# Performance work log

Hardware: AMD Instinct MI355X
Metric: run time of the kernel (lower is better)

The kernel has to match this reference:

```python
import jax, jax.numpy as jnp
import numpy as np

N = 100_000   # nodes
E = 1_600_000 # edges
F = 128       # num_node_features
H = 128       # hidden_channels
C = 10        # num_classes
G = 128       # graphs in batch


def setup_inputs() -> dict:
    key = jax.random.key(0)
    ks = jax.random.split(key, 12)
    x = jax.random.normal(ks[0], (N, F), jnp.float32)
    edge_index = jax.random.randint(ks[1], (2, E), 0, N, dtype=jnp.int32)
    batch = jnp.sort(jax.random.randint(ks[2], (N,), 0, G, dtype=jnp.int32))
    s = 1.0 / np.sqrt(H)
    W0 = jax.random.normal(ks[3], (F, H), jnp.float32) * s
    b0 = jnp.zeros((H,), jnp.float32)
    W1 = jax.random.normal(ks[4], (H, H), jnp.float32) * s
    b1 = jnp.zeros((H,), jnp.float32)
    W2 = jax.random.normal(ks[5], (H, H), jnp.float32) * s
    b2 = jnp.zeros((H,), jnp.float32)
    Wlin = jax.random.normal(ks[6], (H, C), jnp.float32) * s
    blin = jnp.zeros((C,), jnp.float32)
    return {"x": x, "edge_index": edge_index, "batch": batch,
            "W0": W0, "b0": b0, "W1": W1, "b1": b1, "W2": W2, "b2": b2,
            "Wlin": Wlin, "blin": blin}


def gcn_conv(x, W, b, src, dst):
    """PyG GCNConv: symmetric-normalized aggregation with self-loops."""
    xw = x @ W  # [N, H]
    # degree from destination column, +1 for self-loop (gcn_norm)
    deg = jax.ops.segment_sum(jnp.ones(src.shape[0], xw.dtype), dst,
                              num_segments=N) + 1.0
    dinv = jax.lax.rsqrt(deg)  # deg^{-1/2}
    # edge messages: xw[src] * deg_src^{-1/2} * deg_dst^{-1/2}
    msg = xw[src] * (dinv[src] * dinv[dst])[:, None]  # [E, H]
    agg = jax.ops.segment_sum(msg, dst, num_segments=N)
    # self-loop contribution: xw * deg^{-1}
    return agg + xw * (dinv * dinv)[:, None] + b


def reference(x, edge_index, batch, W0, b0, W1, b1, W2, b2, Wlin, blin):
    src, dst = edge_index[0], edge_index[1]
    h = jax.nn.relu(gcn_conv(x, W0, b0, src, dst))
    h = jax.nn.relu(gcn_conv(h, W1, b1, src, dst))
    h = jax.nn.relu(gcn_conv(h, W2, b2, src, dst))
    # global_mean_pool over graph ids
    cnt = jax.ops.segment_sum(jnp.ones(N, h.dtype), batch, num_segments=G)
    pooled = jax.ops.segment_sum(h, batch, num_segments=G) / jnp.maximum(cnt, 1.0)[:, None]
    # dropout is identity in eval mode
    return pooled @ Wlin + blin  # [G, C]
```

## Files before the change

kernel.cpp:

```cpp
#include <hip/hip_runtime.h>

typedef short short8 __attribute__((ext_vector_type(8)));
typedef float f32x4 __attribute__((ext_vector_type(4)));
typedef float f32x2 __attribute__((ext_vector_type(2)));

#define HDIM 128
#define SCAN_NB 256
#define SCAN_TPB 256
#define XCC_GETREG_IMM (20 | (31 << 11))

__device__ __forceinline__ ushort f2bf(float f) {
  uint u = __float_as_uint(f);
  u += 0x7fffu + ((u >> 16) & 1u);
  return (ushort)(u >> 16);
}
__device__ __forceinline__ float bflo(uint v){ return __uint_as_float(v << 16); }
__device__ __forceinline__ float bfhi(uint v){ return __uint_as_float(v & 0xffff0000u); }
__device__ __forceinline__ uchar f2fp8(float f) {
  int p = __builtin_amdgcn_cvt_pk_fp8_f32(f, f, 0, false);
  return (uchar)(p & 0xff);
}

__global__ __launch_bounds__(256) void k_wconv(const float* __restrict__ W0, const float* __restrict__ W1,
    const float* __restrict__ W2, ushort* __restrict__ wf) {
  int b = blockIdx.x;
  const float* W = (b < 8) ? W0 : (b < 16) ? W1 : W2;
  ushort* out = wf + (size_t)(b >> 3) * 16384;
  int g = (b & 7) * 256 + threadIdx.x;
  int nt = g >> 8, kc = (g >> 6) & 3, lane = g & 63;
  int colB = lane & 15, krow = (lane >> 4) * 8;
  ushort v[8];
  #pragma unroll
  for (int j = 0; j < 8; ++j)
    v[j] = f2bf(W[(kc*32 + krow + j)*HDIM + nt*16 + colB]);
  #pragma unroll
  for (int j = 0; j < 8; ++j) out[(size_t)g*8 + j] = v[j];
}

__global__ __launch_bounds__(256) void k_deg(const int* __restrict__ dst, int E, int N,
                                             int* __restrict__ degc8, ushort* __restrict__ rank) {
  uint xcd = __builtin_amdgcn_s_getreg(XCC_GETREG_IMM) & 7u;
  int* plane = degc8 + (size_t)xcd * N;
  for (int e = blockIdx.x*blockDim.x + threadIdx.x; e < E; e += gridDim.x*blockDim.x) {
    int d = dst[e];
    int r = __hip_atomic_fetch_add(&plane[d], 1, __ATOMIC_RELAXED, __HIP_MEMORY_SCOPE_WORKGROUP);
    rank[e] = (ushort)((xcd << 13) | (uint)r);
  }
}

__global__ __launch_bounds__(SCAN_TPB) void k_scanA(const int* __restrict__ degc8, int N,
    int* __restrict__ degc, int* __restrict__ blocksum, float* __restrict__ dinv) {
  int ipt = (N + SCAN_NB*SCAN_TPB - 1) / (SCAN_NB*SCAN_TPB);
  int chunk = ipt * SCAN_TPB;
  int start = blockIdx.x * chunk + threadIdx.x * ipt;
  int s = 0;
  #pragma unroll
  for (int k = 0; k < 4; ++k) {
    if (k < ipt) {
      int i = start + k;
      if (i < N) {
        int d = 0;
        #pragma unroll
        for (int x = 0; x < 8; ++x) d += degc8[(size_t)x*N + i];
        degc[i] = d;
        s += d;
        dinv[i] = rsqrtf((float)d + 1.0f);
      }
    }
  }
  __shared__ int red[SCAN_TPB];
  int t = threadIdx.x;
  red[t] = s; __syncthreads();
  for (int off = SCAN_TPB/2; off > 0; off >>= 1) {
    if (t < off) red[t] += red[t+off];
    __syncthreads();
  }
  if (t == 0) blocksum[blockIdx.x] = red[0];
}

__global__ __launch_bounds__(SCAN_NB) void k_scanB(const int* __restrict__ blocksum,
    int* __restrict__ blockoff, int* __restrict__ totalN,
    const int* __restrict__ batch, int N, int G, float* __restrict__ inv_cnt) {
  int t = threadIdx.x;
  if (blockIdx.x == 0) {
    __shared__ int sh[SCAN_NB];
    sh[t] = blocksum[t];
    __syncthreads();
    for (int off = 1; off < SCAN_NB; off <<= 1) {
      int v = (t >= off) ? sh[t-off] : 0;
      __syncthreads();
      sh[t] += v;
      __syncthreads();
    }
    blockoff[t] = (t == 0) ? 0 : sh[t-1];
    if (t == SCAN_NB-1) *totalN = sh[t];
  } else {
    __shared__ int bnd[SCAN_NB+1];
    if (t <= G) {
      int lo = 0, hi = N;
      while (lo < hi) { int mid = (lo + hi) >> 1; if (batch[mid] < t) lo = mid + 1; else hi = mid; }
      bnd[t] = lo;
    }
    __syncthreads();
    if (t < G) {
      int c = bnd[t+1] - bnd[t];
      inv_cnt[t] = 1.0f / (float)max(c, 1);
    }
  }
}

__global__ __launch_bounds__(SCAN_TPB) void k_scanC(const int* __restrict__ degc,
    const int* __restrict__ degc8, int N,
    const int* __restrict__ blockoff, const int* __restrict__ totalN,
    int* __restrict__ row_ptr, int* __restrict__ row_ptr8) {
  int ipt = (N + SCAN_NB*SCAN_TPB - 1) / (SCAN_NB*SCAN_TPB);
  int chunk = ipt * SCAN_TPB;
  int start = blockIdx.x * chunk + threadIdx.x * ipt;
  int t = threadIdx.x;
  int vals[4];
  int s = 0;
  #pragma unroll
  for (int k = 0; k < 4; ++k) {
    int v = 0;
    if (k < ipt) { int i = start + k; if (i < N) v = degc[i]; }
    vals[k] = v; s += v;
  }
  __shared__ int sh[SCAN_TPB];
  sh[t] = s; __syncthreads();
  for (int off = 1; off < SCAN_TPB; off <<= 1) {
    int v = (t >= off) ? sh[t-off] : 0;
    __syncthreads();
    sh[t] += v;
    __syncthreads();
  }
  int run = blockoff[blockIdx.x] + ((t == 0) ? 0 : sh[t-1]);
  #pragma unroll
  for (int k = 0; k < 4; ++k) {
    if (k < ipt) {
      int i = start + k;
      if (i < N) {
        row_ptr[i] = run;
        int c = run;
        #pragma unroll
        for (int x = 0; x < 8; ++x) {
          row_ptr8[(size_t)x*N + i] = c;
          c += degc8[(size_t)x*N + i];
        }
      }
    }
    run += vals[k];
  }
  if (blockIdx.x == 0 && t == 0) row_ptr[N] = *totalN;
}

__global__ __launch_bounds__(256) void k_fill(const int* __restrict__ src, const int* __restrict__ dst, int E, int N,
    const float* __restrict__ dinv, const int* __restrict__ row_ptr8, const ushort* __restrict__ rank,
    int2* __restrict__ epack) {
  for (int e = blockIdx.x*blockDim.x + threadIdx.x; e < E; e += gridDim.x*blockDim.x) {
    int s = src[e], d = dst[e];
    uint rk = rank[e];
    uint xcd = rk >> 13;
    int  r   = (int)(rk & 0x1FFFu);
    int pos = row_ptr8[(size_t)xcd*N + d] + r;
    float cf = dinv[s] * dinv[d];
    epack[pos] = make_int2(s, __float_as_int(cf));
  }
}

template<int IN_F32>
__global__ __launch_bounds__(256,1) void k_gemm(const void* __restrict__ in_, const ushort* __restrict__ wf,
    uchar* __restrict__ xw8, int N) {
  int lane = threadIdx.x & 63;
  int wid  = (blockIdx.x * blockDim.x + threadIdx.x) >> 6;
  int nw   = (gridDim.x * blockDim.x) >> 6;
  int colB = lane & 15;
  int krow = (lane >> 4) * 8;

  short8 bfr[8][4];
  #pragma unroll
  for (int nt = 0; nt < 8; ++nt)
    #pragma unroll
    for (int kc = 0; kc < 4; ++kc)
      bfr[nt][kc] = *(const short8*)(wf + (((nt<<2) + kc) << 9) + (lane << 3));

  int strips = (N + 15) >> 4;
  for (int s = wid; s < strips; s += nw) {
    int ra = s*16 + colB;
    bool va = ra < N;
    short8 a[4];
    if (IN_F32) {
      const float* xin = (const float*)in_;
      #pragma unroll
      for (int kc = 0; kc < 4; ++kc) {
        short8 t = {0,0,0,0,0,0,0,0};
        if (va) {
          const float* p = xin + (size_t)ra*HDIM + kc*32 + krow;
          float4 lo4 = *(const float4*)p;
          float4 hi4 = *(const float4*)(p+4);
          t[0]=(short)f2bf(lo4.x); t[1]=(short)f2bf(lo4.y); t[2]=(short)f2bf(lo4.z); t[3]=(short)f2bf(lo4.w);
          t[4]=(short)f2bf(hi4.x); t[5]=(short)f2bf(hi4.y); t[6]=(short)f2bf(hi4.z); t[7]=(short)f2bf(hi4.w);
        }
        a[kc] = t;
      }
    } else {
      const ushort* hin = (const ushort*)in_;
      #pragma unroll
      for (int kc = 0; kc < 4; ++kc) {
        short8 t = {0,0,0,0,0,0,0,0};
        if (va) t = *(const short8*)(hin + (size_t)ra*HDIM + kc*32 + krow);
        a[kc] = t;
      }
    }
    f32x4 acc[8];
    #pragma unroll
    for (int nt = 0; nt < 8; ++nt) { acc[nt][0]=0.f; acc[nt][1]=0.f; acc[nt][2]=0.f; acc[nt][3]=0.f; }
    #pragma unroll
    for (int nt = 0; nt < 8; ++nt)
      #pragma unroll
      for (int kc = 0; kc < 4; ++kc)
        acc[nt] = __builtin_amdgcn_mfma_f32_16x16x32_bf16(a[kc], bfr[nt][kc], acc[nt], 0, 0, 0);

    int r0 = s*16 + (lane>>4)*4;
    #pragma unroll
    for (int nt = 0; nt < 8; ++nt) {
      int c = nt*16 + colB;
      #pragma unroll
      for (int rg = 0; rg < 4; ++rg) {
        int rr = r0 + rg;
        if (rr < N) xw8[(size_t)rr*HDIM + c] = f2fp8(acc[nt][rg]);
      }
    }
  }
}

__global__ __launch_bounds__(256) void k_agg(const ushort* __restrict__ xw8u, const int2* __restrict__ epack,
    const int* __restrict__ row_ptr, const float* __restrict__ dinv, const float* __restrict__ bias,
    uint* __restrict__ hu, int N) {
  int lane = threadIdx.x & 63;
  int n = blockIdx.x*4 + (threadIdx.x >> 6);
  if (n >= N) return;
  int e0 = row_ptr[n], e1 = row_ptr[n+1];
  float a0 = 0.f, a1 = 0.f;
  for (int base = e0; base < e1; base += 64) {
    int cnt = min(64, e1 - base);
    int2 myp = make_int2(0, 0);
    if (lane < cnt) myp = epack[base + lane];
    for (int j = 0; j < cnt; j += 16) {
      #pragma unroll
      for (int u = 0; u < 16; ++u) {
        int idx = j + u;
        int   sN = __shfl(myp.x, idx);
        float cf = __int_as_float(__shfl(myp.y, idx));
        int v16 = (int)xw8u[(size_t)sN*64 + lane];
        f32x2 f = __builtin_amdgcn_cvt_pk_f32_fp8(v16, false);
        a0 += cf * f[0];
        a1 += cf * f[1];
      }
    }
  }
  float di = dinv[n]; float w = di*di;
  int v16s = (int)xw8u[(size_t)n*64 + lane];
  f32x2 fs = __builtin_amdgcn_cvt_pk_f32_fp8(v16s, false);
  a0 += w * fs[0];
  a1 += w * fs[1];
  a0 += bias[lane*2];  a1 += bias[lane*2+1];
  a0 = fmaxf(a0, 0.f); a1 = fmaxf(a1, 0.f);
  uint o = ((uint)f2bf(a0)) | (((uint)f2bf(a1)) << 16);
  hu[(size_t)n*64 + lane] = o;
}

__global__ __launch_bounds__(256) void k_pool(const uint* __restrict__ hu, const int* __restrict__ batch,
    float* __restrict__ psum, int N) {
  int lane = threadIdx.x & 63;
  int wave = threadIdx.x >> 6;
  int n0 = blockIdx.x*512 + wave*128;
  if (n0 >= N) return;
  int n1 = min(n0 + 128, N);
  float a0 = 0.f, a1 = 0.f;
  int gc = batch[n0];
  for (int n = n0; n < n1; ++n) {
    int g = batch[n];
    if (g != gc) {
      atomicAdd(&psum[gc*HDIM + lane*2],   a0);
      atomicAdd(&psum[gc*HDIM + lane*2+1], a1);
      a0 = 0.f; a1 = 0.f; gc = g;
    }
    uint v = hu[(size_t)n*64 + lane];
    a0 += bflo(v); a1 += bfhi(v);
  }
  atomicAdd(&psum[gc*HDIM + lane*2],   a0);
  atomicAdd(&psum[gc*HDIM + lane*2+1], a1);
}

__global__ __launch_bounds__(256) void k_final(const float* __restrict__ psum, const float* __restrict__ inv_cnt,
    const float* __restrict__ Wlin, const float* __restrict__ blin, float* __restrict__ out, int G, int C) {
  int idx = blockIdx.x*256 + threadIdx.x;
  if (idx >= G*C) return;
  int g = idx / C, c = idx % C;
  float acc = 0.f;
  for (int k = 0; k < HDIM; ++k) acc += psum[g*HDIM + k] * Wlin[k*C + c];
  out[idx] = acc * inv_cnt[g] + blin[c];
}

extern "C" void kernel_launch(void* const* d_in, const int* in_sizes, int n_in,
                              void* d_out, int out_size, void* d_ws, size_t ws_size,
                              hipStream_t stream) {
  const float* x    = (const float*)d_in[0];
  const int*   ei   = (const int*)d_in[1];
  const int*   batch= (const int*)d_in[2];
  const float* W0   = (const float*)d_in[3];
  const float* b0   = (const float*)d_in[4];
  const float* W1   = (const float*)d_in[5];
  const float* b1   = (const float*)d_in[6];
  const float* W2   = (const float*)d_in[7];
  const float* b2   = (const float*)d_in[8];
  const float* Wlin = (const float*)d_in[9];
  const float* blin = (const float*)d_in[10];

  int N = in_sizes[0] / HDIM;
  int E = in_sizes[1] / 2;
  int C = in_sizes[10];
  int G = out_size / C;
  const int* src = ei;
  const int* dst = ei + E;

  char* ws = (char*)d_ws;
  size_t o = 0;
  auto alloc = [&](size_t bytes){ size_t r = o; o += (bytes + 511) & ~(size_t)511; return r; };
  size_t zbeg  = o;
  int*    degc8   = (int*)   (ws + alloc((size_t)8*N*4));
  float*  psum    = (float*) (ws + alloc((size_t)G*HDIM*4));
  size_t zend  = o;
  int*    degc    = (int*)   (ws + alloc((size_t)N*4));
  float*  dinv    = (float*) (ws + alloc((size_t)N*4));
  int*    row_ptr = (int*)   (ws + alloc((size_t)(N+1)*4));
  int*    row_ptr8= (int*)   (ws + alloc((size_t)8*N*4));
  float*  inv_cnt = (float*) (ws + alloc((size_t)G*4));
  int*    blocksum= (int*)   (ws + alloc((size_t)SCAN_NB*4));
  int*    blockoff= (int*)   (ws + alloc((size_t)SCAN_NB*4));
  int*    totalN  = (int*)   (ws + alloc(4));
  ushort* wf      = (ushort*)(ws + alloc((size_t)3*16384*2));
  ushort* rank    = (ushort*)(ws + alloc((size_t)E*2));
  int2*   epack   = (int2*)  (ws + alloc((size_t)E*8));
  uchar*  xw8     = (uchar*) (ws + alloc((size_t)N*HDIM));
  ushort* hbuf    = (ushort*)(ws + alloc((size_t)N*HDIM*2));

  hipMemsetAsync(ws + zbeg, 0, zend - zbeg, stream);

  k_wconv<<<24, 256, 0, stream>>>(W0, W1, W2, wf);
  k_deg  <<<2048, 256, 0, stream>>>(dst, E, N, degc8, rank);
  k_scanA<<<SCAN_NB, SCAN_TPB, 0, stream>>>(degc8, N, degc, blocksum, dinv);
  k_scanB<<<2, SCAN_NB, 0, stream>>>(blocksum, blockoff, totalN, batch, N, G, inv_cnt);
  k_scanC<<<SCAN_NB, SCAN_TPB, 0, stream>>>(degc, degc8, N, blockoff, totalN, row_ptr, row_ptr8);
  k_fill <<<2048, 256, 0, stream>>>(src, dst, E, N, dinv, row_ptr8, rank, epack);

  const int gemm_blocks = 512;
  const int agg_blocks  = (N + 3) / 4;

  k_gemm<1><<<gemm_blocks, 256, 0, stream>>>((const void*)x, wf, xw8, N);
  k_agg<<<agg_blocks, 256, 0, stream>>>((const ushort*)xw8, epack, row_ptr, dinv, b0, (uint*)hbuf, N);
  k_gemm<0><<<gemm_blocks, 256, 0, stream>>>((const void*)hbuf, wf + 16384, xw8, N);
  k_agg<<<agg_blocks, 256, 0, stream>>>((const ushort*)xw8, epack, row_ptr, dinv, b1, (uint*)hbuf, N);
  k_gemm<0><<<gemm_blocks, 256, 0, stream>>>((const void*)hbuf, wf + 32768, xw8, N);
  k_agg<<<agg_blocks, 256, 0, stream>>>((const ushort*)xw8, epack, row_ptr, dinv, b2, (uint*)hbuf, N);

  k_pool<<<(N + 511)/512, 256, 0, stream>>>((const uint*)hbuf, batch, psum, N);
  k_final<<<(G*C + 255)/256, 256, 0, stream>>>(psum, inv_cnt, Wlin, blin, (float*)d_out, G, C);
}
```

Measured before the change: 365.4 us.

## Fuse first-layer GEMM with degree counting in one heterogeneous launch

The first-layer x@W0 GEMM is merged into the degree-counting kernel: one in four blocks runs the GEMM, converting W0 to bf16 on the fly, while the rest do the atomic degree and rank pass. The aim is to overlap the compute-bound GEMM with the atomic-bound degree pass and remove a separate launch. W0 no longer goes through the weight conversion kernel. The risk is that only 512 blocks do the GEMM while sharing CUs with atomic traffic, and the degree work is spread over fewer blocks.

```diff
diff --git a/kernel.cpp b/kernel.cpp
--- a/kernel.cpp
+++ b/kernel.cpp
@@ -21,10 +21,10 @@
   return (uchar)(p & 0xff);
 }
 
-__global__ __launch_bounds__(256) void k_wconv(const float* __restrict__ W0, const float* __restrict__ W1,
-    const float* __restrict__ W2, ushort* __restrict__ wf) {
+__global__ __launch_bounds__(256) void k_wconv(const float* __restrict__ W1, const float* __restrict__ W2,
+    ushort* __restrict__ wf) {
   int b = blockIdx.x;
-  const float* W = (b < 8) ? W0 : (b < 16) ? W1 : W2;
+  const float* W = (b < 8) ? W1 : W2;
   ushort* out = wf + (size_t)(b >> 3) * 16384;
   int g = (b & 7) * 256 + threadIdx.x;
   int nt = g >> 8, kc = (g >> 6) & 3, lane = g & 63;
@@ -37,14 +37,76 @@
   for (int j = 0; j < 8; ++j) out[(size_t)g*8 + j] = v[j];
 }
 
-__global__ __launch_bounds__(256) void k_deg(const int* __restrict__ dst, int E, int N,
-                                             int* __restrict__ degc8, ushort* __restrict__ rank) {
-  uint xcd = __builtin_amdgcn_s_getreg(XCC_GETREG_IMM) & 7u;
-  int* plane = degc8 + (size_t)xcd * N;
-  for (int e = blockIdx.x*blockDim.x + threadIdx.x; e < E; e += gridDim.x*blockDim.x) {
-    int d = dst[e];
-    int r = __hip_atomic_fetch_add(&plane[d], 1, __ATOMIC_RELAXED, __HIP_MEMORY_SCOPE_WORKGROUP);
-    rank[e] = (ushort)((xcd << 13) | (uint)r);
+__global__ __launch_bounds__(256,1) void k_dg0(const float* __restrict__ xin, const float* __restrict__ W,
+    uchar* __restrict__ xw8, int N,
+    const int* __restrict__ dst, int E, int* __restrict__ degc8, ushort* __restrict__ rank) {
+  if ((blockIdx.x & 3) == 0) {
+    int lane = threadIdx.x & 63;
+    int gb   = blockIdx.x >> 2;
+    int wid  = (gb * 256 + (int)threadIdx.x) >> 6;
+    int nw   = ((gridDim.x >> 2) * 256) >> 6;
+    int colB = lane & 15;
+    int krow = (lane >> 4) * 8;
+
+    short8 bfr[8][4];
+    #pragma unroll
+    for (int nt = 0; nt < 8; ++nt)
+      #pragma unroll
+      for (int kc = 0; kc < 4; ++kc) {
+        short8 t;
+        #pragma unroll
+        for (int j = 0; j < 8; ++j)
+          t[j] = (short)f2bf(W[(kc*32 + krow + j)*HDIM + nt*16 + colB]);
+        bfr[nt][kc] = t;
+      }
+
+    int strips = (N + 15) >> 4;
+    for (int s = wid; s < strips; s += nw) {
+      int ra = s*16 + colB;
+      bool va = ra < N;
+      short8 a[4];
+      #pragma unroll
+      for (int kc = 0; kc < 4; ++kc) {
+        short8 t = {0,0,0,0,0,0,0,0};
+        if (va) {
+          const float* p = xin + (size_t)ra*HDIM + kc*32 + krow;
+          float4 lo4 = *(const float4*)p;
+          float4 hi4 = *(const float4*)(p+4);
+          t[0]=(short)f2bf(lo4.x); t[1]=(short)f2bf(lo4.y); t[2]=(short)f2bf(lo4.z); t[3]=(short)f2bf(lo4.w);
+          t[4]=(short)f2bf(hi4.x); t[5]=(short)f2bf(hi4.y); t[6]=(short)f2bf(hi4.z); t[7]=(short)f2bf(hi4.w);
+        }
+        a[kc] = t;
+      }
+      f32x4 acc[8];
+      #pragma unroll
+      for (int nt = 0; nt < 8; ++nt) { acc[nt][0]=0.f; acc[nt][1]=0.f; acc[nt][2]=0.f; acc[nt][3]=0.f; }
+      #pragma unroll
+      for (int nt = 0; nt < 8; ++nt)
+        #pragma unroll
+        for (int kc = 0; kc < 4; ++kc)
+          acc[nt] = __builtin_amdgcn_mfma_f32_16x16x32_bf16(a[kc], bfr[nt][kc], acc[nt], 0, 0, 0);
+
+      int r0 = s*16 + (lane>>4)*4;
+      #pragma unroll
+      for (int nt = 0; nt < 8; ++nt) {
+        int c = nt*16 + colB;
+        #pragma unroll
+        for (int rg = 0; rg < 4; ++rg) {
+          int rr = r0 + rg;
+          if (rr < N) xw8[(size_t)rr*HDIM + c] = f2fp8(acc[nt][rg]);
+        }
+      }
+    }
+  } else {
+    uint xcd = __builtin_amdgcn_s_getreg(XCC_GETREG_IMM) & 7u;
+    int* plane = degc8 + (size_t)xcd * N;
+    int fb  = blockIdx.x - ((blockIdx.x + 3) >> 2);
+    int nfb = gridDim.x - (gridDim.x >> 2);
+    for (int e = fb*256 + (int)threadIdx.x; e < E; e += nfb*256) {
+      int d = dst[e];
+      int r = __hip_atomic_fetch_add(&plane[d], 1, __ATOMIC_RELAXED, __HIP_MEMORY_SCOPE_WORKGROUP);
+      rank[e] = (ushort)((xcd << 13) | (uint)r);
+    }
   }
 }
 
@@ -167,8 +229,7 @@
   }
 }
 
-template<int IN_F32>
-__global__ __launch_bounds__(256,1) void k_gemm(const void* __restrict__ in_, const ushort* __restrict__ wf,
+__global__ __launch_bounds__(256,1) void k_gemm(const ushort* __restrict__ hin, const ushort* __restrict__ wf,
     uchar* __restrict__ xw8, int N) {
   int lane = threadIdx.x & 63;
   int wid  = (blockIdx.x * blockDim.x + threadIdx.x) >> 6;
@@ -188,28 +249,11 @@
     int ra = s*16 + colB;
     bool va = ra < N;
     short8 a[4];
-    if (IN_F32) {
-      const float* xin = (const float*)in_;
-      #pragma unroll
-      for (int kc = 0; kc < 4; ++kc) {
-        short8 t = {0,0,0,0,0,0,0,0};
-        if (va) {
-          const float* p = xin + (size_t)ra*HDIM + kc*32 + krow;
-          float4 lo4 = *(const float4*)p;
-          float4 hi4 = *(const float4*)(p+4);
-          t[0]=(short)f2bf(lo4.x); t[1]=(short)f2bf(lo4.y); t[2]=(short)f2bf(lo4.z); t[3]=(short)f2bf(lo4.w);
-          t[4]=(short)f2bf(hi4.x); t[5]=(short)f2bf(hi4.y); t[6]=(short)f2bf(hi4.z); t[7]=(short)f2bf(hi4.w);
-        }
-        a[kc] = t;
-      }
-    } else {
-      const ushort* hin = (const ushort*)in_;
-      #pragma unroll
-      for (int kc = 0; kc < 4; ++kc) {
-        short8 t = {0,0,0,0,0,0,0,0};
-        if (va) t = *(const short8*)(hin + (size_t)ra*HDIM + kc*32 + krow);
-        a[kc] = t;
-      }
+    #pragma unroll
+    for (int kc = 0; kc < 4; ++kc) {
+      short8 t = {0,0,0,0,0,0,0,0};
+      if (va) t = *(const short8*)(hin + (size_t)ra*HDIM + kc*32 + krow);
+      a[kc] = t;
     }
     f32x4 acc[8];
     #pragma unroll
@@ -339,7 +383,7 @@
   int*    blocksum= (int*)   (ws + alloc((size_t)SCAN_NB*4));
   int*    blockoff= (int*)   (ws + alloc((size_t)SCAN_NB*4));
   int*    totalN  = (int*)   (ws + alloc(4));
-  ushort* wf      = (ushort*)(ws + alloc((size_t)3*16384*2));
+  ushort* wf      = (ushort*)(ws + alloc((size_t)2*16384*2));
   ushort* rank    = (ushort*)(ws + alloc((size_t)E*2));
   int2*   epack   = (int2*)  (ws + alloc((size_t)E*8));
   uchar*  xw8     = (uchar*) (ws + alloc((size_t)N*HDIM));
@@ -347,8 +391,8 @@
 
   hipMemsetAsync(ws + zbeg, 0, zend - zbeg, stream);
 
-  k_wconv<<<24, 256, 0, stream>>>(W0, W1, W2, wf);
-  k_deg  <<<2048, 256, 0, stream>>>(dst, E, N, degc8, rank);
+  k_wconv<<<16, 256, 0, stream>>>(W1, W2, wf);
+  k_dg0 <<<2048, 256, 0, stream>>>(x, W0, xw8, N, dst, E, degc8, rank);
   k_scanA<<<SCAN_NB, SCAN_TPB, 0, stream>>>(degc8, N, degc, blocksum, dinv);
   k_scanB<<<2, SCAN_NB, 0, stream>>>(blocksum, blockoff, totalN, batch, N, G, inv_cnt);
   k_scanC<<<SCAN_NB, SCAN_TPB, 0, stream>>>(degc, degc8, N, blockoff, totalN, row_ptr, row_ptr8);
@@ -357,11 +401,10 @@
   const int gemm_blocks = 512;
   const int agg_blocks  = (N + 3) / 4;
 
-  k_gemm<1><<<gemm_blocks, 256, 0, stream>>>((const void*)x, wf, xw8, N);
   k_agg<<<agg_blocks, 256, 0, stream>>>((const ushort*)xw8, epack, row_ptr, dinv, b0, (uint*)hbuf, N);
-  k_gemm<0><<<gemm_blocks, 256, 0, stream>>>((const void*)hbuf, wf + 16384, xw8, N);
+  k_gemm<<<gemm_blocks, 256, 0, stream>>>(hbuf, wf, xw8, N);
   k_agg<<<agg_blocks, 256, 0, stream>>>((const ushort*)xw8, epack, row_ptr, dinv, b1, (uint*)hbuf, N);
-  k_gemm<0><<<gemm_blocks, 256, 0, stream>>>((const void*)hbuf, wf + 32768, xw8, N);
+  k_gemm<<<gemm_blocks, 256, 0, stream>>>(hbuf, wf + 16384, xw8, N);
   k_agg<<<agg_blocks, 256, 0, stream>>>((const ushort*)xw8, epack, row_ptr, dinv, b2, (uint*)hbuf, N);
 
   k_pool<<<(N + 511)/512, 256, 0, stream>>>((const uint*)hbuf, batch, psum, N);
```

Result: slower. 383.4 us (+4.9%).
